# Kernel tuning notes

Measured on AMD Instinct MI355X. Metric: run time of the kernel, lower is better.

Reference implementation:

```python
import jax, jax.numpy as jnp
import numpy as np

N_NODES = 100000
N_EDGES = 320000
HID = 256
NE = 128  # node_embed_dim = hid // 2 (use_stats=True, sgrl=False)
N_LAYERS = 3

NET, DEV, PIN = 0, 1, 2


def setup_inputs() -> dict:
    key = jax.random.key(0)
    ks = jax.random.split(key, 24)
    s = 0.05
    inp = {
        "node_attr": jax.random.uniform(ks[0], (N_NODES, 17), dtype=jnp.float32),
        "y": jax.random.uniform(ks[1], (N_NODES, 2), dtype=jnp.float32),
        "node_emb": jax.random.normal(ks[2], (4, NE), dtype=jnp.float32) * s,
        "edge_emb": jax.random.normal(ks[3], (4, HID), dtype=jnp.float32) * s,
        "net_W": jax.random.normal(ks[4], (17, NE), dtype=jnp.float32) * s,
        "net_b": jnp.zeros((NE,), jnp.float32),
        "dev_W": jax.random.normal(ks[5], (17, NE), dtype=jnp.float32) * s,
        "dev_b": jnp.zeros((NE,), jnp.float32),
        "pin_emb": jax.random.normal(ks[6], (17, NE), dtype=jnp.float32) * s,
        "sage_Wl": jax.random.normal(ks[7], (N_LAYERS, HID, HID), dtype=jnp.float32) * s,
        "sage_bl": jnp.zeros((N_LAYERS, HID), jnp.float32),
        "sage_Wr": jax.random.normal(ks[8], (N_LAYERS, HID, HID), dtype=jnp.float32) * s,
        "head_W0": jax.random.normal(ks[9], (HID, HID), dtype=jnp.float32) * s,
        "head_b0": jnp.zeros((HID,), jnp.float32),
        "head_W1": jax.random.normal(ks[10], (HID, 1), dtype=jnp.float32) * s,
        "head_b1": jnp.zeros((1,), jnp.float32),
        "node_type": jax.random.randint(ks[11], (N_NODES,), 0, 4, dtype=jnp.int32),
        "edge_type": jax.random.randint(ks[12], (N_EDGES,), 0, 4, dtype=jnp.int32),
        "edge_index": jax.random.randint(ks[13], (2, N_EDGES), 0, N_NODES, dtype=jnp.int32),
    }
    return inp


def _forward(node_attr, y, node_emb, edge_emb, net_W, net_b, dev_W, dev_b,
             pin_emb, sage_Wl, sage_bl, sage_Wr, head_W0, head_b0, head_W1,
             head_b1, node_type, edge_type, edge_index):
    # node / edge type encoders (embedding lookups)
    x = node_emb[node_type]                 # [N, NE]
    xe = edge_emb[edge_type]                # [N_E, HID] (unused by SAGE, kept for fidelity)
    del xe

    # per-type attribute embedding, scattered into a zero tensor via disjoint masks
    net_mask = node_type == NET
    dev_mask = node_type == DEV
    pin_mask = node_type == PIN
    net_e = node_attr @ net_W + net_b       # [N, NE]
    dev_e = node_attr @ dev_W + dev_b       # [N, NE]
    pin_idx = node_attr[:, 0].astype(jnp.int32)
    pin_e = pin_emb[pin_idx]                # [N, NE]
    attr_emb = jnp.where(net_mask[:, None], net_e,
                jnp.where(dev_mask[:, None], dev_e,
                jnp.where(pin_mask[:, None], pin_e, jnp.zeros_like(net_e))))
    x = jnp.concatenate([x, attr_emb], axis=1)  # [N, HID]

    src, dst = edge_index[0], edge_index[1]
    cnt = jax.ops.segment_sum(jnp.ones_like(src, dtype=x.dtype), dst,
                              num_segments=N_NODES)
    denom = jnp.maximum(cnt, 1.0)[:, None]
    for l in range(N_LAYERS):
        # SAGEConv: mean-aggregate neighbor features, then two linear maps
        agg = jax.ops.segment_sum(x[src], dst, num_segments=N_NODES) / denom
        x = agg @ sage_Wl[l] + sage_bl[l] + x @ sage_Wr[l]
        x = jax.nn.relu(x)

    # head MLP (2 layers): Linear -> ReLU -> Linear
    h = jax.nn.relu(x @ head_W0 + head_b0)
    pred = h @ head_W1 + head_b1            # [N, 1]
    true_class = y[:, 1].astype(jnp.int32)
    true_label = y
    return pred, true_class, true_label


def reference(node_attr, y, node_emb, edge_emb, net_W, net_b, dev_W, dev_b,
              pin_emb, sage_Wl, sage_bl, sage_Wr, head_W0, head_b0, head_W1,
              head_b1, node_type, edge_type, edge_index):
    return _forward(node_attr, y, node_emb, edge_emb, net_W, net_b, dev_W,
                    dev_b, pin_emb, sage_Wl, sage_bl, sage_Wr, head_W0,
                    head_b0, head_W1, head_b1, node_type, edge_type,
                    edge_index)
```

## Files before the change

kernel.cpp:

```cpp
#include <hip/hip_runtime.h>
#include <hip/hip_bf16.h>

#define N_NODES 100000
#define N_EDGES 320000
#define HID 256
#define NE 128
#define NLAYERS 3

typedef __attribute__((ext_vector_type(8))) short short8;
typedef __attribute__((ext_vector_type(4))) float f32x4;

__device__ inline float bfbits2f(unsigned int b) { return __uint_as_float(b << 16); }

__device__ inline unsigned int pack_bf2(float lo, float hi) {
    __hip_bfloat16 l = __float2bfloat16(lo), h = __float2bfloat16(hi);
    return (unsigned int)*(unsigned short*)&l |
           ((unsigned int)*(unsigned short*)&h << 16);
}

__global__ __launch_bounds__(256) void k_prep(
    const float* __restrict__ Wl, const float* __restrict__ Wr,
    const float* __restrict__ W0,
    __hip_bfloat16* __restrict__ Wt, __hip_bfloat16* __restrict__ Wh,
    int* __restrict__ deg, int* __restrict__ total)
{
    int t = blockIdx.x * 256 + threadIdx.x;
    const int total_sage = 3 * 256 * 512;
    if (t < total_sage) {
        int l = t >> 17;
        int rem = t & 131071;
        int n = rem >> 9;
        int k = rem & 511;
        const float* Wsrc = (k < 256) ? (Wl + (size_t)l * 65536)
                                      : (Wr + (size_t)l * 65536);
        Wt[t] = __float2bfloat16(Wsrc[(k & 255) * 256 + n]);
    } else {
        int u = t - total_sage;
        if (u < 65536) {
            int n = u >> 8, k = u & 255;
            Wh[u] = __float2bfloat16(W0[k * 256 + n]);
        }
    }
    if (t < N_NODES) deg[t] = 0;
    if (t == 0) *total = 0;
}

__global__ __launch_bounds__(256) void k_init(
    const float* __restrict__ node_attr,
    const float* __restrict__ node_emb,
    const float* __restrict__ net_W, const float* __restrict__ net_b,
    const float* __restrict__ dev_W, const float* __restrict__ dev_b,
    const float* __restrict__ pin_emb,
    const int*   __restrict__ node_type,
    const float* __restrict__ y, const float* __restrict__ b1,
    const int*   __restrict__ edge_index, int* __restrict__ deg,
    float* __restrict__ out,
    __hip_bfloat16* __restrict__ x)
{
    int t = blockIdx.x * 256 + threadIdx.x;
    if (t < N_NODES * 32) {
        int n  = t >> 5;
        int c4 = (t & 31) * 4;
        int ty = node_type[n];
        float4 e = *(const float4*)(node_emb + ty * NE + c4);
        float4 a;
        if (ty == 0 || ty == 1) {
            const float* W = (ty == 0) ? net_W : dev_W;
            const float* b = (ty == 0) ? net_b : dev_b;
            a = *(const float4*)(b + c4);
            const float* ar = node_attr + (size_t)n * 17;
            #pragma unroll
            for (int k = 0; k < 17; ++k) {
                float av = ar[k];
                float4 wv = *(const float4*)(W + k * NE + c4);
                a.x += av * wv.x; a.y += av * wv.y;
                a.z += av * wv.z; a.w += av * wv.w;
            }
        } else if (ty == 2) {
            int idx = (int)node_attr[(size_t)n * 17];
            a = *(const float4*)(pin_emb + idx * NE + c4);
        } else {
            a.x = a.y = a.z = a.w = 0.0f;
        }
        uint2 ev = {pack_bf2(e.x, e.y), pack_bf2(e.z, e.w)};
        uint2 av = {pack_bf2(a.x, a.y), pack_bf2(a.z, a.w)};
        *(uint2*)((char*)x + (size_t)n * 512 + c4 * 2)       = ev;
        *(uint2*)((char*)x + (size_t)n * 512 + 256 + c4 * 2) = av;
    } else if (t < N_NODES * 33) {
        int n = t - N_NODES * 32;
        float y0 = y[(size_t)n * 2 + 0];
        float y1 = y[(size_t)n * 2 + 1];
        out[n] = b1[0];
        out[N_NODES + n] = (float)(int)y1;
        out[2 * N_NODES + 2 * n + 0] = y0;
        out[2 * N_NODES + 2 * n + 1] = y1;
    } else {
        int e = t - N_NODES * 33;
        if (e < N_EDGES) atomicAdd(&deg[edge_index[N_EDGES + e]], 1);
    }
}

__global__ __launch_bounds__(256) void k_alloc(
    const int* __restrict__ deg, int* __restrict__ off,
    int* __restrict__ cursor, int* __restrict__ total)
{
    int n = blockIdx.x * 256 + threadIdx.x;
    int lane = threadIdx.x & 63;
    int d = (n < N_NODES) ? deg[n] : 0;
    int incl = d;
    #pragma unroll
    for (int o = 1; o < 64; o <<= 1) {
        int v = __shfl_up(incl, o, 64);
        if (lane >= o) incl += v;
    }
    int wtot = __shfl(incl, 63, 64);
    int base = 0;
    if (lane == 63) base = atomicAdd(total, wtot);
    base = __shfl(base, 63, 64);
    if (n < N_NODES) {
        int o = base + incl - d;
        off[n] = o;
        cursor[n] = o;
    }
}

__global__ __launch_bounds__(256) void k_fill(
    const int* __restrict__ edge_index, int* __restrict__ cursor,
    int* __restrict__ slots)
{
    int e = blockIdx.x * 256 + threadIdx.x;
    if (e >= N_EDGES) return;
    int s = edge_index[e];
    int d = edge_index[N_EDGES + e];
    int slot = atomicAdd(&cursor[d], 1);
    slots[slot] = s;
}

__global__ __launch_bounds__(256) void k_aggregate(
    const __hip_bfloat16* __restrict__ x,
    const int* __restrict__ off, const int* __restrict__ deg,
    const int* __restrict__ slots,
    __hip_bfloat16* __restrict__ agg)
{
    int g = blockIdx.x * 256 + threadIdx.x;
    int wid = g >> 6;
    int lane = g & 63;
    int sub = lane >> 4;
    int l16 = lane & 15;
    int n = wid * 4 + sub;
    bool active = n < N_NODES;
    int o = 0, d = 0;
    if (active) { o = off[n]; d = deg[n]; }
    float acc[16];
    #pragma unroll
    for (int i = 0; i < 16; ++i) acc[i] = 0.0f;
    for (int p = 0; p < d; ++p) {
        int src = slots[o + p];
        const char* rp = (const char*)x + (size_t)src * 512 + l16 * 32;
        uint4 v0 = *(const uint4*)rp;
        uint4 v1 = *(const uint4*)(rp + 16);
        const unsigned int u[8] = {v0.x, v0.y, v0.z, v0.w, v1.x, v1.y, v1.z, v1.w};
        #pragma unroll
        for (int i = 0; i < 8; ++i) {
            acc[2 * i + 0] += bfbits2f(u[i] & 0xffffu);
            acc[2 * i + 1] += __uint_as_float(u[i] & 0xffff0000u);
        }
    }
    if (active) {
        float rs = 1.0f / fmaxf((float)d, 1.0f);
        unsigned int w[8];
        #pragma unroll
        for (int i = 0; i < 8; ++i)
            w[i] = pack_bf2(acc[2 * i + 0] * rs, acc[2 * i + 1] * rs);
        uint4 o0 = {w[0], w[1], w[2], w[3]};
        uint4 o1 = {w[4], w[5], w[6], w[7]};
        char* op = (char*)agg + (size_t)n * 512 + l16 * 32;
        *(uint4*)op = o0;
        *(uint4*)(op + 16) = o1;
    }
}

template <bool SAGE>
__global__ __launch_bounds__(512, 4) void k_mfma(
    const __hip_bfloat16* __restrict__ Agg,
    const __hip_bfloat16* __restrict__ X,
    const __hip_bfloat16* __restrict__ Wt,
    const float* __restrict__ bias,
    const float* __restrict__ W1,
    __hip_bfloat16* __restrict__ Out,
    float* __restrict__ Pred)
{
    __shared__ char As[3][16384];

    const int tid  = threadIdx.x;
    const int w    = tid >> 6, lane = tid & 63;
    const int l15  = lane & 15, lg = lane >> 4;
    const int row0 = blockIdx.x * 128;
    const int KT     = SAGE ? 512 : 256;
    const int nsteps = SAGE ? 8 : 4;

    f32x4 acc[8][2];
    #pragma unroll
    for (int i = 0; i < 8; ++i)
        #pragma unroll
        for (int n = 0; n < 2; ++n) acc[i][n] = (f32x4)0.0f;

    const int srow   = tid >> 3;
    const int schunk = tid & 7;

    auto stage = [&](int s) {
        const int b = s % 3;
        const char* base;
        int k0;
        if (SAGE && s < 4) { base = (const char*)Agg; k0 = s * 64; }
        else               { base = (const char*)X;   k0 = (SAGE ? s - 4 : s) * 64; }
        #pragma unroll
        for (int issue = 0; issue < 2; ++issue) {
            int row  = srow + issue * 64;
            int grow = row0 + row;
            if (grow >= N_NODES) grow = N_NODES - 1;
            const char* gp = base + (size_t)grow * 512 + (size_t)k0 * 2
                           + ((schunk ^ (row & 7)) << 4);
            const char* lp = &As[b][issue * 8192 + tid * 16];
            __builtin_amdgcn_global_load_lds(
                (const __attribute__((address_space(1))) void*)gp,
                (__attribute__((address_space(3))) void*)lp, 16, 0, 0);
        }
    };

    auto loadB = [&](int s, short8 (&bb)[2][2]) {
        #pragma unroll
        for (int h = 0; h < 2; ++h)
            #pragma unroll
            for (int n = 0; n < 2; ++n) {
                int c = w * 32 + n * 16 + l15;
                bb[h][n] = *(const short8*)(Wt + (size_t)c * KT + s * 64 + h * 32 + 8 * lg);
            }
    };

    auto do_step = [&](int s, bool last, short8 (&bcur)[2][2], short8 (&bnxt)[2][2]) {
        const int b = s % 3;
        if (last) asm volatile("s_waitcnt vmcnt(0)" ::: "memory");
        else      asm volatile("s_waitcnt vmcnt(2)" ::: "memory");
        __builtin_amdgcn_sched_barrier(0);
        __builtin_amdgcn_s_barrier();
        __builtin_amdgcn_sched_barrier(0);
        if (!last) loadB(s + 1, bnxt);
        if (s + 2 < nsteps) stage(s + 2);
        #pragma unroll
        for (int h = 0; h < 2; ++h) {
            #pragma unroll
            for (int i = 0; i < 8; ++i) {
                int r = i * 16 + l15;
                short8 a = *(const short8*)&As[b][r * 128 + (((lg + 4 * h) ^ (r & 7)) << 4)];
                acc[i][0] = __builtin_amdgcn_mfma_f32_16x16x32_bf16(a, bcur[h][0], acc[i][0], 0, 0, 0);
                acc[i][1] = __builtin_amdgcn_mfma_f32_16x16x32_bf16(a, bcur[h][1], acc[i][1], 0, 0, 0);
            }
        }
    };

    short8 b0[2][2], b1[2][2];
    loadB(0, b0);
    stage(0);
    stage(1);
    if (SAGE) {
        do_step(0, false, b0, b1);
        do_step(1, false, b1, b0);
        do_step(2, false, b0, b1);
        do_step(3, false, b1, b0);
        do_step(4, false, b0, b1);
        do_step(5, false, b1, b0);
        do_step(6, false, b0, b1);
        do_step(7, true,  b1, b0);
    } else {
        do_step(0, false, b0, b1);
        do_step(1, false, b1, b0);
        do_step(2, false, b0, b1);
        do_step(3, true,  b1, b0);
    }

    if (SAGE) {
        __syncthreads();
        __hip_bfloat16* lo = (__hip_bfloat16*)As;
        #pragma unroll
        for (int hh = 0; hh < 2; ++hh) {
            #pragma unroll
            for (int n = 0; n < 2; ++n) {
                int c = w * 32 + n * 16 + l15;
                float bv = bias[c];
                #pragma unroll
                for (int i2 = 0; i2 < 4; ++i2) {
                    int i = hh * 4 + i2;
                    #pragma unroll
                    for (int r = 0; r < 4; ++r) {
                        int rl = i2 * 16 + lg * 4 + r;
                        lo[rl * 256 + c] = __float2bfloat16(fmaxf(acc[i][n][r] + bv, 0.0f));
                    }
                }
            }
            __syncthreads();
            #pragma unroll
            for (int q = 0; q < 4; ++q) {
                int chunk = tid + q * 512;
                int rl = chunk >> 5, cc = chunk & 31;
                int grow = row0 + hh * 64 + rl;
                if (grow < N_NODES)
                    *(uint4*)((char*)Out + (size_t)grow * 512 + cc * 16) =
                        *(const uint4*)((const char*)As + rl * 512 + cc * 16);
            }
            __syncthreads();
        }
    } else {
        #pragma unroll
        for (int i = 0; i < 8; ++i) {
            float p[4];
            #pragma unroll
            for (int r = 0; r < 4; ++r) p[r] = 0.0f;
            #pragma unroll
            for (int n = 0; n < 2; ++n) {
                int c = w * 32 + n * 16 + l15;
                float bv = bias[c];
                float wv = W1[c];
                #pragma unroll
                for (int r = 0; r < 4; ++r)
                    p[r] += fmaxf(acc[i][n][r] + bv, 0.0f) * wv;
            }
            #pragma unroll
            for (int r = 0; r < 4; ++r) {
                float s = p[r];
                #pragma unroll
                for (int m = 1; m < 16; m <<= 1) s += __shfl_xor(s, m, 64);
                if (l15 == 0) {
                    int row = row0 + i * 16 + lg * 4 + r;
                    if (row < N_NODES) atomicAdd(&Pred[row], s);
                }
            }
        }
    }
}

extern "C" void kernel_launch(void* const* d_in, const int* in_sizes, int n_in,
                              void* d_out, int out_size, void* d_ws, size_t ws_size,
                              hipStream_t stream) {
    const float* node_attr = (const float*)d_in[0];
    const float* y         = (const float*)d_in[1];
    const float* node_emb  = (const float*)d_in[2];
    const float* net_W     = (const float*)d_in[4];
    const float* net_b     = (const float*)d_in[5];
    const float* dev_W     = (const float*)d_in[6];
    const float* dev_b     = (const float*)d_in[7];
    const float* pin_emb   = (const float*)d_in[8];
    const float* sage_Wl   = (const float*)d_in[9];
    const float* sage_bl   = (const float*)d_in[10];
    const float* sage_Wr   = (const float*)d_in[11];
    const float* head_W0   = (const float*)d_in[12];
    const float* head_b0   = (const float*)d_in[13];
    const float* head_W1   = (const float*)d_in[14];
    const float* head_b1   = (const float*)d_in[15];
    const int*   node_type = (const int*)d_in[16];
    const int*   edge_idx  = (const int*)d_in[18];
    float* out = (float*)d_out;

    const size_t xelems = (size_t)N_NODES * HID;
    char* p = (char*)d_ws;
    __hip_bfloat16* x0  = (__hip_bfloat16*)p;  p += xelems * 2;
    __hip_bfloat16* x1  = (__hip_bfloat16*)p;  p += xelems * 2;
    __hip_bfloat16* agg = (__hip_bfloat16*)p;  p += xelems * 2;
    __hip_bfloat16* Wt  = (__hip_bfloat16*)p;  p += (size_t)3 * 256 * 512 * 2;
    __hip_bfloat16* Wh  = (__hip_bfloat16*)p;  p += (size_t)256 * 256 * 2;
    int* deg    = (int*)p; p += N_NODES * 4;
    int* off    = (int*)p; p += N_NODES * 4;
    int* cursor = (int*)p; p += N_NODES * 4;
    int* slots  = (int*)p; p += N_EDGES * 4;
    int* total  = (int*)p; p += 16;

    k_prep<<<(3 * 131072 + 65536 + 255) / 256, 256, 0, stream>>>(
        sage_Wl, sage_Wr, head_W0, Wt, Wh, deg, total);
    k_init<<<(N_NODES * 33 + N_EDGES + 255) / 256, 256, 0, stream>>>(
        node_attr, node_emb, net_W, net_b, dev_W, dev_b, pin_emb, node_type,
        y, head_b1, edge_idx, deg, out, x0);
    k_alloc<<<(N_NODES + 255) / 256, 256, 0, stream>>>(deg, off, cursor, total);
    k_fill<<<(N_EDGES + 255) / 256, 256, 0, stream>>>(edge_idx, cursor, slots);

    const int gemm_grid = (N_NODES + 127) / 128;
    __hip_bfloat16* xcur = x0;
    __hip_bfloat16* xalt = x1;
    for (int l = 0; l < NLAYERS; ++l) {
        k_aggregate<<<(N_NODES / 4 * 64 + 255) / 256, 256, 0, stream>>>(
            xcur, off, deg, slots, agg);
        k_mfma<true><<<gemm_grid, 512, 0, stream>>>(
            agg, xcur, Wt + (size_t)l * 131072,
            sage_bl + (size_t)l * HID, nullptr, xalt, nullptr);
        __hip_bfloat16* t = xcur; xcur = xalt; xalt = t;
    }
    k_mfma<false><<<gemm_grid, 512, 0, stream>>>(
        xcur, xcur, Wh, head_b0, head_W1, nullptr, out);
}
```

Measured before the change: 361.7 us.

## Shrink GEMM tiles to 64 rows by 128 columns with 256-thread blocks

Retiles the fused SAGE/head MFMA GEMM. Each block now covers 64 rows and half of the 256 output columns with 4 waves, where before it covered 128 rows and all columns with 8 waves. The aim is more, smaller blocks for better occupancy and load balance, using a new LDS swizzle and a single-pass epilogue. The cost is that every A tile is now loaded twice, once per column half, which doubles A global traffic. The head reduction also now does twice as many atomic adds into Pred.

```diff
diff --git a/kernel.cpp b/kernel.cpp
--- a/kernel.cpp
+++ b/kernel.cpp
@@ -181,7 +181,7 @@
 }
 
 template <bool SAGE>
-__global__ __launch_bounds__(512, 4) void k_mfma(
+__global__ __launch_bounds__(256, 8) void k_mfma(
     const __hip_bfloat16* __restrict__ Agg,
     const __hip_bfloat16* __restrict__ X,
     const __hip_bfloat16* __restrict__ Wt,
@@ -190,23 +190,27 @@
     __hip_bfloat16* __restrict__ Out,
     float* __restrict__ Pred)
 {
-    __shared__ char As[3][16384];
+    __shared__ char As[3][8192];
 
     const int tid  = threadIdx.x;
     const int w    = tid >> 6, lane = tid & 63;
     const int l15  = lane & 15, lg = lane >> 4;
-    const int row0 = blockIdx.x * 128;
+    const int row0 = (blockIdx.x >> 1) * 64;
+    const int ch   = blockIdx.x & 1;
+    const int col0 = ch * 128 + w * 32;
     const int KT     = SAGE ? 512 : 256;
     const int nsteps = SAGE ? 8 : 4;
 
-    f32x4 acc[8][2];
+    f32x4 acc[4][2];
     #pragma unroll
-    for (int i = 0; i < 8; ++i)
+    for (int i = 0; i < 4; ++i)
         #pragma unroll
         for (int n = 0; n < 2; ++n) acc[i][n] = (f32x4)0.0f;
 
-    const int srow   = tid >> 3;
-    const int schunk = tid & 7;
+    const int srow = tid >> 2;
+    const int clow = tid & 3;
+    int sgrow = row0 + srow; if (sgrow >= N_NODES) sgrow = N_NODES - 1;
+    const int rho  = (srow >> 1) & 3;
 
     auto stage = [&](int s) {
         const int b = s % 3;
@@ -216,12 +220,10 @@
         else               { base = (const char*)X;   k0 = (SAGE ? s - 4 : s) * 64; }
         #pragma unroll
         for (int issue = 0; issue < 2; ++issue) {
-            int row  = srow + issue * 64;
-            int grow = row0 + row;
-            if (grow >= N_NODES) grow = N_NODES - 1;
-            const char* gp = base + (size_t)grow * 512 + (size_t)k0 * 2
-                           + ((schunk ^ (row & 7)) << 4);
-            const char* lp = &As[b][issue * 8192 + tid * 16];
+            int slot = clow + issue * 4;
+            int g    = slot ^ rho;
+            const char* gp = base + (size_t)sgrow * 512 + (size_t)k0 * 2 + g * 16;
+            const char* lp = &As[b][issue * 4096 + tid * 16];
             __builtin_amdgcn_global_load_lds(
                 (const __attribute__((address_space(1))) void*)gp,
                 (__attribute__((address_space(3))) void*)lp, 16, 0, 0);
@@ -233,7 +235,7 @@
         for (int h = 0; h < 2; ++h)
             #pragma unroll
             for (int n = 0; n < 2; ++n) {
-                int c = w * 32 + n * 16 + l15;
+                int c = col0 + n * 16 + l15;
                 bb[h][n] = *(const short8*)(Wt + (size_t)c * KT + s * 64 + h * 32 + 8 * lg);
             }
     };
@@ -250,9 +252,10 @@
         #pragma unroll
         for (int h = 0; h < 2; ++h) {
             #pragma unroll
-            for (int i = 0; i < 8; ++i) {
-                int r = i * 16 + l15;
-                short8 a = *(const short8*)&As[b][r * 128 + (((lg + 4 * h) ^ (r & 7)) << 4)];
+            for (int i = 0; i < 4; ++i) {
+                int r  = i * 16 + l15;
+                int sl = (h * 4 + lg) ^ ((r >> 1) & 3);
+                short8 a = *(const short8*)&As[b][(sl >> 2) * 4096 + r * 64 + (sl & 3) * 16];
                 acc[i][0] = __builtin_amdgcn_mfma_f32_16x16x32_bf16(a, bcur[h][0], acc[i][0], 0, 0, 0);
                 acc[i][1] = __builtin_amdgcn_mfma_f32_16x16x32_bf16(a, bcur[h][1], acc[i][1], 0, 0, 0);
             }
@@ -283,44 +286,38 @@
         __syncthreads();
         __hip_bfloat16* lo = (__hip_bfloat16*)As;
         #pragma unroll
-        for (int hh = 0; hh < 2; ++hh) {
+        for (int n = 0; n < 2; ++n) {
+            int cl = w * 32 + n * 16 + l15;
+            float bv = bias[col0 + n * 16 + l15];
+            #pragma unroll
+            for (int i = 0; i < 4; ++i)
+                #pragma unroll
+                for (int r = 0; r < 4; ++r) {
+                    int rl = i * 16 + lg * 4 + r;
+                    lo[rl * 128 + cl] = __float2bfloat16(fmaxf(acc[i][n][r] + bv, 0.0f));
+                }
+        }
+        __syncthreads();
+        #pragma unroll
+        for (int q = 0; q < 4; ++q) {
+            int chunk = tid + q * 256;
+            int rl = chunk >> 4, cc = chunk & 15;
+            int grow = row0 + rl;
+            if (grow < N_NODES)
+                *(uint4*)((char*)Out + (size_t)grow * 512 + ch * 256 + cc * 16) =
+                    *(const uint4*)((const char*)As + rl * 256 + cc * 16);
+        }
+    } else {
+        #pragma unroll
+        for (int i = 0; i < 4; ++i) {
+            float p[4];
+            #pragma unroll
+            for (int r = 0; r < 4; ++r) p[r] = 0.0f;
             #pragma unroll
             for (int n = 0; n < 2; ++n) {
-                int c = w * 32 + n * 16 + l15;
-                float bv = bias[c];
-                #pragma unroll
-                for (int i2 = 0; i2 < 4; ++i2) {
-                    int i = hh * 4 + i2;
-                    #pragma unroll
-                    for (int r = 0; r < 4; ++r) {
-                        int rl = i2 * 16 + lg * 4 + r;
-                        lo[rl * 256 + c] = __float2bfloat16(fmaxf(acc[i][n][r] + bv, 0.0f));
-                    }
-                }
-            }
-            __syncthreads();
-            #pragma unroll
-            for (int q = 0; q < 4; ++q) {
-                int chunk = tid + q * 512;
-                int rl = chunk >> 5, cc = chunk & 31;
-                int grow = row0 + hh * 64 + rl;
-                if (grow < N_NODES)
-                    *(uint4*)((char*)Out + (size_t)grow * 512 + cc * 16) =
-                        *(const uint4*)((const char*)As + rl * 512 + cc * 16);
-            }
-            __syncthreads();
-        }
-    } else {
-        #pragma unroll
-        for (int i = 0; i < 8; ++i) {
-            float p[4];
-            #pragma unroll
-            for (int r = 0; r < 4; ++r) p[r] = 0.0f;
-            #pragma unroll
-            for (int n = 0; n < 2; ++n) {
-                int c = w * 32 + n * 16 + l15;
-                float bv = bias[c];
-                float wv = W1[c];
+                int cg = col0 + n * 16 + l15;
+                float bv = bias[cg];
+                float wv = W1[cg];
                 #pragma unroll
                 for (int r = 0; r < 4; ++r)
                     p[r] += fmaxf(acc[i][n][r] + bv, 0.0f) * wv;
@@ -382,17 +379,17 @@
     k_alloc<<<(N_NODES + 255) / 256, 256, 0, stream>>>(deg, off, cursor, total);
     k_fill<<<(N_EDGES + 255) / 256, 256, 0, stream>>>(edge_idx, cursor, slots);
 
-    const int gemm_grid = (N_NODES + 127) / 128;
+    const int gemm_grid = ((N_NODES + 63) / 64) * 2;
     __hip_bfloat16* xcur = x0;
     __hip_bfloat16* xalt = x1;
     for (int l = 0; l < NLAYERS; ++l) {
         k_aggregate<<<(N_NODES / 4 * 64 + 255) / 256, 256, 0, stream>>>(
             xcur, off, deg, slots, agg);
-        k_mfma<true><<<gemm_grid, 512, 0, stream>>>(
+        k_mfma<true><<<gemm_grid, 256, 0, stream>>>(
             agg, xcur, Wt + (size_t)l * 131072,
             sage_bl + (size_t)l * HID, nullptr, xalt, nullptr);
         __hip_bfloat16* t = xcur; xcur = xalt; xalt = t;
     }
-    k_mfma<false><<<gemm_grid, 512, 0, stream>>>(
+    k_mfma<false><<<gemm_grid, 256, 0, stream>>>(
         xcur, xcur, Wh, head_b0, head_W1, nullptr, out);
 }
```

New measurement: 403.7 us. +11.6%, slower.

## Fuse head MLP into final SAGE layer GEMM kernel

Applied to the files above, without the earlier changes.

The last SAGE layer's output tile is kept in LDS as bf16 and fed directly into the head W0 GEMM and the W1 dot product inside the same kernel. This removes one kernel launch and the write and re-read of the final 100k×256 activation. Per-wave partial predictions are also reduced in shared memory and written directly, with b1 added there, replacing the atomicAdd into a pre-initialised output. The fused kernel uses 64KB of LDS, which may lower occupancy below the launch-bounds target of four blocks.

```diff
diff --git a/kernel.cpp b/kernel.cpp
--- a/kernel.cpp
+++ b/kernel.cpp
@@ -180,161 +180,218 @@
     }
 }
 
-template <bool SAGE>
-__global__ __launch_bounds__(512, 4) void k_mfma(
+#define SAGE_KLOOP(SMEM)                                                      \
+    const int tid  = threadIdx.x;                                             \
+    const int w    = tid >> 6, lane = tid & 63;                               \
+    const int l15  = lane & 15, lg = lane >> 4;                               \
+    const int row0 = blockIdx.x * 128;                                        \
+    f32x4 acc[8][2];                                                          \
+    _Pragma("unroll")                                                         \
+    for (int i = 0; i < 8; ++i)                                               \
+        _Pragma("unroll")                                                     \
+        for (int n = 0; n < 2; ++n) acc[i][n] = (f32x4)0.0f;                  \
+    const int srow   = tid >> 3;                                              \
+    const int schunk = tid & 7;                                               \
+    auto stage = [&](int s) {                                                 \
+        const int b = s % 3;                                                  \
+        const char* base;                                                     \
+        int k0;                                                               \
+        if (s < 4) { base = (const char*)Agg; k0 = s * 64; }                  \
+        else       { base = (const char*)X;   k0 = (s - 4) * 64; }            \
+        _Pragma("unroll")                                                     \
+        for (int issue = 0; issue < 2; ++issue) {                             \
+            int row  = srow + issue * 64;                                     \
+            int grow = row0 + row;                                            \
+            if (grow >= N_NODES) grow = N_NODES - 1;                          \
+            const char* gp = base + (size_t)grow * 512 + (size_t)k0 * 2       \
+                           + ((schunk ^ (row & 7)) << 4);                     \
+            const char* lp = SMEM + b * 16384 + issue * 8192 + tid * 16;      \
+            __builtin_amdgcn_global_load_lds(                                 \
+                (const __attribute__((address_space(1))) void*)gp,            \
+                (__attribute__((address_space(3))) void*)lp, 16, 0, 0);       \
+        }                                                                     \
+    };                                                                        \
+    auto loadB = [&](int s, short8 (&bb)[2][2]) {                             \
+        _Pragma("unroll")                                                     \
+        for (int h = 0; h < 2; ++h)                                           \
+            _Pragma("unroll")                                                 \
+            for (int n = 0; n < 2; ++n) {                                     \
+                int c = w * 32 + n * 16 + l15;                                \
+                bb[h][n] = *(const short8*)(Wt + (size_t)c * 512 + s * 64     \
+                                            + h * 32 + 8 * lg);               \
+            }                                                                 \
+    };                                                                        \
+    auto do_step = [&](int s, bool last, short8 (&bcur)[2][2],                \
+                       short8 (&bnxt)[2][2]) {                                \
+        const int b = s % 3;                                                  \
+        if (last) asm volatile("s_waitcnt vmcnt(0)" ::: "memory");            \
+        else      asm volatile("s_waitcnt vmcnt(2)" ::: "memory");            \
+        __builtin_amdgcn_sched_barrier(0);                                    \
+        __builtin_amdgcn_s_barrier();                                         \
+        __builtin_amdgcn_sched_barrier(0);                                    \
+        if (!last) loadB(s + 1, bnxt);                                        \
+        if (s + 2 < 8) stage(s + 2);                                          \
+        _Pragma("unroll")                                                     \
+        for (int h = 0; h < 2; ++h) {                                         \
+            _Pragma("unroll")                                                 \
+            for (int i = 0; i < 8; ++i) {                                     \
+                int r = i * 16 + l15;                                         \
+                short8 a = *(const short8*)(SMEM + b * 16384 + r * 128        \
+                                + (((lg + 4 * h) ^ (r & 7)) << 4));           \
+                acc[i][0] = __builtin_amdgcn_mfma_f32_16x16x32_bf16(          \
+                    a, bcur[h][0], acc[i][0], 0, 0, 0);                       \
+                acc[i][1] = __builtin_amdgcn_mfma_f32_16x16x32_bf16(          \
+                    a, bcur[h][1], acc[i][1], 0, 0, 0);                       \
+            }                                                                 \
+        }                                                                     \
+    };                                                                        \
+    short8 b0[2][2], b1r[2][2];                                               \
+    loadB(0, b0);                                                             \
+    stage(0);                                                                 \
+    stage(1);                                                                 \
+    do_step(0, false, b0, b1r);                                               \
+    do_step(1, false, b1r, b0);                                               \
+    do_step(2, false, b0, b1r);                                               \
+    do_step(3, false, b1r, b0);                                               \
+    do_step(4, false, b0, b1r);                                               \
+    do_step(5, false, b1r, b0);                                               \
+    do_step(6, false, b0, b1r);                                               \
+    do_step(7, true,  b1r, b0);
+
+__global__ __launch_bounds__(512, 4) void k_sage(
     const __hip_bfloat16* __restrict__ Agg,
     const __hip_bfloat16* __restrict__ X,
     const __hip_bfloat16* __restrict__ Wt,
     const float* __restrict__ bias,
+    __hip_bfloat16* __restrict__ Out)
+{
+    __shared__ char smem[49152];
+    SAGE_KLOOP(smem)
+
+    __syncthreads();
+    __hip_bfloat16* lo = (__hip_bfloat16*)smem;
+    #pragma unroll
+    for (int hh = 0; hh < 2; ++hh) {
+        #pragma unroll
+        for (int n = 0; n < 2; ++n) {
+            int c = w * 32 + n * 16 + l15;
+            float bv = bias[c];
+            #pragma unroll
+            for (int i2 = 0; i2 < 4; ++i2) {
+                int i = hh * 4 + i2;
+                #pragma unroll
+                for (int r = 0; r < 4; ++r) {
+                    int rl = i2 * 16 + lg * 4 + r;
+                    lo[rl * 256 + c] = __float2bfloat16(fmaxf(acc[i][n][r] + bv, 0.0f));
+                }
+            }
+        }
+        __syncthreads();
+        #pragma unroll
+        for (int q = 0; q < 4; ++q) {
+            int chunk = tid + q * 512;
+            int rl = chunk >> 5, cc = chunk & 31;
+            int grow = row0 + hh * 64 + rl;
+            if (grow < N_NODES)
+                *(uint4*)((char*)Out + (size_t)grow * 512 + cc * 16) =
+                    *(const uint4*)((const char*)smem + rl * 512 + cc * 16);
+        }
+        __syncthreads();
+    }
+}
+
+__global__ __launch_bounds__(512, 4) void k_sage3(
+    const __hip_bfloat16* __restrict__ Agg,
+    const __hip_bfloat16* __restrict__ X,
+    const __hip_bfloat16* __restrict__ Wt,
+    const float* __restrict__ bias,
+    const __hip_bfloat16* __restrict__ Wh,
+    const float* __restrict__ hb0,
     const float* __restrict__ W1,
-    __hip_bfloat16* __restrict__ Out,
+    const float* __restrict__ b1,
     float* __restrict__ Pred)
 {
-    __shared__ char As[3][16384];
-
-    const int tid  = threadIdx.x;
-    const int w    = tid >> 6, lane = tid & 63;
-    const int l15  = lane & 15, lg = lane >> 4;
-    const int row0 = blockIdx.x * 128;
-    const int KT     = SAGE ? 512 : 256;
-    const int nsteps = SAGE ? 8 : 4;
-
-    f32x4 acc[8][2];
+    __shared__ char smem[65536];
+    SAGE_KLOOP(smem)
+
+    __syncthreads();
+    #pragma unroll
+    for (int n = 0; n < 2; ++n) {
+        int c = w * 32 + n * 16 + l15;
+        float bv = bias[c];
+        int chunk = c >> 3;
+        int chi = chunk & 24, clo = chunk & 7;
+        #pragma unroll
+        for (int i = 0; i < 8; ++i)
+            #pragma unroll
+            for (int r = 0; r < 4; ++r) {
+                int row = i * 16 + lg * 4 + r;
+                __hip_bfloat16 hv = __float2bfloat16(fmaxf(acc[i][n][r] + bv, 0.0f));
+                *(short*)(smem + row * 512 + (chi | (clo ^ (row & 7))) * 16
+                          + (c & 7) * 2) = *(short*)&hv;
+            }
+    }
+    __syncthreads();
+
+    f32x4 hacc[8][2];
     #pragma unroll
     for (int i = 0; i < 8; ++i)
         #pragma unroll
-        for (int n = 0; n < 2; ++n) acc[i][n] = (f32x4)0.0f;
-
-    const int srow   = tid >> 3;
-    const int schunk = tid & 7;
-
-    auto stage = [&](int s) {
-        const int b = s % 3;
-        const char* base;
-        int k0;
-        if (SAGE && s < 4) { base = (const char*)Agg; k0 = s * 64; }
-        else               { base = (const char*)X;   k0 = (SAGE ? s - 4 : s) * 64; }
-        #pragma unroll
-        for (int issue = 0; issue < 2; ++issue) {
-            int row  = srow + issue * 64;
-            int grow = row0 + row;
-            if (grow >= N_NODES) grow = N_NODES - 1;
-            const char* gp = base + (size_t)grow * 512 + (size_t)k0 * 2
-                           + ((schunk ^ (row & 7)) << 4);
-            const char* lp = &As[b][issue * 8192 + tid * 16];
-            __builtin_amdgcn_global_load_lds(
-                (const __attribute__((address_space(1))) void*)gp,
-                (__attribute__((address_space(3))) void*)lp, 16, 0, 0);
-        }
-    };
-
-    auto loadB = [&](int s, short8 (&bb)[2][2]) {
-        #pragma unroll
-        for (int h = 0; h < 2; ++h)
+        for (int n = 0; n < 2; ++n) hacc[i][n] = (f32x4)0.0f;
+    #pragma unroll
+    for (int ks = 0; ks < 4; ++ks) {
+        #pragma unroll
+        for (int h = 0; h < 2; ++h) {
+            short8 bb[2];
             #pragma unroll
             for (int n = 0; n < 2; ++n) {
                 int c = w * 32 + n * 16 + l15;
-                bb[h][n] = *(const short8*)(Wt + (size_t)c * KT + s * 64 + h * 32 + 8 * lg);
+                bb[n] = *(const short8*)(Wh + (size_t)c * 256 + ks * 64 + h * 32 + 8 * lg);
             }
-    };
-
-    auto do_step = [&](int s, bool last, short8 (&bcur)[2][2], short8 (&bnxt)[2][2]) {
-        const int b = s % 3;
-        if (last) asm volatile("s_waitcnt vmcnt(0)" ::: "memory");
-        else      asm volatile("s_waitcnt vmcnt(2)" ::: "memory");
-        __builtin_amdgcn_sched_barrier(0);
-        __builtin_amdgcn_s_barrier();
-        __builtin_amdgcn_sched_barrier(0);
-        if (!last) loadB(s + 1, bnxt);
-        if (s + 2 < nsteps) stage(s + 2);
-        #pragma unroll
-        for (int h = 0; h < 2; ++h) {
             #pragma unroll
             for (int i = 0; i < 8; ++i) {
                 int r = i * 16 + l15;
-                short8 a = *(const short8*)&As[b][r * 128 + (((lg + 4 * h) ^ (r & 7)) << 4)];
-                acc[i][0] = __builtin_amdgcn_mfma_f32_16x16x32_bf16(a, bcur[h][0], acc[i][0], 0, 0, 0);
-                acc[i][1] = __builtin_amdgcn_mfma_f32_16x16x32_bf16(a, bcur[h][1], acc[i][1], 0, 0, 0);
+                int swz = ks * 8 + ((h * 4 + lg) ^ (r & 7));
+                short8 a = *(const short8*)(smem + r * 512 + swz * 16);
+                hacc[i][0] = __builtin_amdgcn_mfma_f32_16x16x32_bf16(a, bb[0], hacc[i][0], 0, 0, 0);
+                hacc[i][1] = __builtin_amdgcn_mfma_f32_16x16x32_bf16(a, bb[1], hacc[i][1], 0, 0, 0);
             }
         }
-    };
-
-    short8 b0[2][2], b1[2][2];
-    loadB(0, b0);
-    stage(0);
-    stage(1);
-    if (SAGE) {
-        do_step(0, false, b0, b1);
-        do_step(1, false, b1, b0);
-        do_step(2, false, b0, b1);
-        do_step(3, false, b1, b0);
-        do_step(4, false, b0, b1);
-        do_step(5, false, b1, b0);
-        do_step(6, false, b0, b1);
-        do_step(7, true,  b1, b0);
-    } else {
-        do_step(0, false, b0, b1);
-        do_step(1, false, b1, b0);
-        do_step(2, false, b0, b1);
-        do_step(3, true,  b1, b0);
-    }
-
-    if (SAGE) {
-        __syncthreads();
-        __hip_bfloat16* lo = (__hip_bfloat16*)As;
-        #pragma unroll
-        for (int hh = 0; hh < 2; ++hh) {
-            #pragma unroll
-            for (int n = 0; n < 2; ++n) {
-                int c = w * 32 + n * 16 + l15;
-                float bv = bias[c];
-                #pragma unroll
-                for (int i2 = 0; i2 < 4; ++i2) {
-                    int i = hh * 4 + i2;
-                    #pragma unroll
-                    for (int r = 0; r < 4; ++r) {
-                        int rl = i2 * 16 + lg * 4 + r;
-                        lo[rl * 256 + c] = __float2bfloat16(fmaxf(acc[i][n][r] + bv, 0.0f));
-                    }
-                }
-            }
-            __syncthreads();
-            #pragma unroll
-            for (int q = 0; q < 4; ++q) {
-                int chunk = tid + q * 512;
-                int rl = chunk >> 5, cc = chunk & 31;
-                int grow = row0 + hh * 64 + rl;
-                if (grow < N_NODES)
-                    *(uint4*)((char*)Out + (size_t)grow * 512 + cc * 16) =
-                        *(const uint4*)((const char*)As + rl * 512 + cc * 16);
-            }
-            __syncthreads();
-        }
-    } else {
-        #pragma unroll
-        for (int i = 0; i < 8; ++i) {
-            float p[4];
-            #pragma unroll
-            for (int r = 0; r < 4; ++r) p[r] = 0.0f;
-            #pragma unroll
-            for (int n = 0; n < 2; ++n) {
-                int c = w * 32 + n * 16 + l15;
-                float bv = bias[c];
-                float wv = W1[c];
-                #pragma unroll
-                for (int r = 0; r < 4; ++r)
-                    p[r] += fmaxf(acc[i][n][r] + bv, 0.0f) * wv;
-            }
-            #pragma unroll
-            for (int r = 0; r < 4; ++r) {
-                float s = p[r];
-                #pragma unroll
-                for (int m = 1; m < 16; m <<= 1) s += __shfl_xor(s, m, 64);
-                if (l15 == 0) {
-                    int row = row0 + i * 16 + lg * 4 + r;
-                    if (row < N_NODES) atomicAdd(&Pred[row], s);
-                }
-            }
+    }
+    __syncthreads();
+
+    float* part = (float*)smem;
+    #pragma unroll
+    for (int i = 0; i < 8; ++i) {
+        float p[4];
+        #pragma unroll
+        for (int r = 0; r < 4; ++r) p[r] = 0.0f;
+        #pragma unroll
+        for (int n = 0; n < 2; ++n) {
+            int cg = w * 32 + n * 16 + l15;
+            float bv = hb0[cg];
+            float wv = W1[cg];
+            #pragma unroll
+            for (int r = 0; r < 4; ++r)
+                p[r] += fmaxf(hacc[i][n][r] + bv, 0.0f) * wv;
+        }
+        #pragma unroll
+        for (int r = 0; r < 4; ++r) {
+            float s = p[r];
+            #pragma unroll
+            for (int m = 1; m < 16; m <<= 1) s += __shfl_xor(s, m, 64);
+            if (l15 == 0)
+                part[(i * 16 + lg * 4 + r) * 8 + w] = s;
+        }
+    }
+    __syncthreads();
+    if (tid < 128) {
+        int grow = row0 + tid;
+        if (grow < N_NODES) {
+            float s = b1[0];
+            #pragma unroll
+            for (int j = 0; j < 8; ++j) s += part[tid * 8 + j];
+            Pred[grow] = s;
         }
     }
 }
@@ -383,16 +440,17 @@
     k_fill<<<(N_EDGES + 255) / 256, 256, 0, stream>>>(edge_idx, cursor, slots);
 
     const int gemm_grid = (N_NODES + 127) / 128;
-    __hip_bfloat16* xcur = x0;
-    __hip_bfloat16* xalt = x1;
-    for (int l = 0; l < NLAYERS; ++l) {
-        k_aggregate<<<(N_NODES / 4 * 64 + 255) / 256, 256, 0, stream>>>(
-            xcur, off, deg, slots, agg);
-        k_mfma<true><<<gemm_grid, 512, 0, stream>>>(
-            agg, xcur, Wt + (size_t)l * 131072,
-            sage_bl + (size_t)l * HID, nullptr, xalt, nullptr);
-        __hip_bfloat16* t = xcur; xcur = xalt; xalt = t;
-    }
-    k_mfma<false><<<gemm_grid, 512, 0, stream>>>(
-        xcur, xcur, Wh, head_b0, head_W1, nullptr, out);
-}
+    k_aggregate<<<(N_NODES / 4 * 64 + 255) / 256, 256, 0, stream>>>(
+        x0, off, deg, slots, agg);
+    k_sage<<<gemm_grid, 512, 0, stream>>>(
+        agg, x0, Wt, sage_bl, x1);
+    k_aggregate<<<(N_NODES / 4 * 64 + 255) / 256, 256, 0, stream>>>(
+        x1, off, deg, slots, agg);
+    k_sage<<<gemm_grid, 512, 0, stream>>>(
+        agg, x1, Wt + 131072, sage_bl + HID, x0);
+    k_aggregate<<<(N_NODES / 4 * 64 + 255) / 256, 256, 0, stream>>>(
+        x0, off, deg, slots, agg);
+    k_sage3<<<gemm_grid, 512, 0, stream>>>(
+        agg, x0, Wt + 2 * 131072, sage_bl + 2 * HID,
+        Wh, head_b0, head_W1, head_b1, out);
+}
```

After: 361.4 us. About the same (-0.1%).
